# Performance work log

Hardware: AMD Instinct MI355X
Metric: run time of the kernel (lower is better)

The kernel has to match this reference:

```python
import jax, jax.numpy as jnp
import numpy as np

N_VOXELS = 262144
MAX_PTS = 32
C = 4
N_PATCHES = 2048          # total patches across the batch
VOXELS_PER_PATCH = 128    # N_PATCHES * 128 == N_VOXELS
BATCH = 4
PATCH_PER_SAMPLE = 512    # BATCH * 512 == N_PATCHES


def setup_inputs() -> dict:
    key = jax.random.key(0)
    k1, k2, k3, k4 = jax.random.split(key, 4)
    patch_voxels = jax.random.normal(k1, (N_VOXELS, MAX_PTS, C), dtype=jnp.float32)
    patch_voxel_num_points = jax.random.randint(k2, (N_VOXELS,), 0, MAX_PTS + 1, dtype=jnp.int32)
    patch_voxel_coords = jax.random.randint(k3, (N_VOXELS, 4), 0, 256, dtype=jnp.int32)
    # counts per patch; must sum to N_VOXELS (constant counts for a fixed-shape reference)
    patch_voxel_num_array = jnp.ones((N_PATCHES,), dtype=jnp.int32) * VOXELS_PER_PATCH
    valid_patch_center_array = jax.random.normal(k4, (N_PATCHES, 2), dtype=jnp.float32)
    valid_patch_num_array = jnp.ones((BATCH,), dtype=jnp.int32) * PATCH_PER_SAMPLE
    return {
        'patch_voxels': patch_voxels,
        'patch_voxel_num_points': patch_voxel_num_points,
        'patch_voxel_coords': patch_voxel_coords,
        'patch_voxel_num_array': patch_voxel_num_array,
        'valid_patch_center_array': valid_patch_center_array,
        'valid_patch_num_array': valid_patch_num_array,
    }


def reference(patch_voxels, patch_voxel_num_points, patch_voxel_coords,
              patch_voxel_num_array, valid_patch_center_array, valid_patch_num_array):
    # --- voxel mean pooling: sum over points, divide by clamped point count ---
    points_sum = patch_voxels.sum(axis=1)                                  # [N, C]
    normalizer = jnp.clip(patch_voxel_num_points.astype(patch_voxels.dtype), 1.0)[:, None]
    voxel_features = points_sum / normalizer                               # [N, C]

    # --- vectorized segment-id assignment (replaces the per-patch Python loop) ---
    # voxel j belongs to patch i where cumsum[i-1] <= j < cumsum[i]
    accu = jnp.cumsum(patch_voxel_num_array)                               # [P]
    n = patch_voxels.shape[0]
    batch_ids = jnp.searchsorted(accu, jnp.arange(n, dtype=accu.dtype), side='right')
    voxel_coords = patch_voxel_coords.at[:, 0].set(batch_ids.astype(patch_voxel_coords.dtype))

    # --- patch centers padded with z = 0 (flat array instead of per-sample list) ---
    z_pad = jnp.zeros((valid_patch_center_array.shape[0], 1), dtype=jnp.float32)
    patch_center_xyz = jnp.concatenate([valid_patch_center_array, z_pad], axis=-1)  # [V, 3]

    patch_num_list = valid_patch_num_array.astype(jnp.int32)
    return voxel_features, voxel_coords, patch_center_xyz, patch_num_list
```

## Files before the change

kernel.cpp:

```cpp
#include <hip/hip_runtime.h>


#define P_MAX 4096

__device__ __forceinline__ void reduce_store(
    float4 a0, float4 a1, float4 a2, float4 a3,
    int np, int t, int voxel, float4* __restrict__ out0)
{
    float sx = a0.x + a1.x + a2.x + a3.x;
    float sy = a0.y + a1.y + a2.y + a3.y;
    float sz = a0.z + a1.z + a2.z + a3.z;
    float sw = a0.w + a1.w + a2.w + a3.w;
#pragma unroll
    for (int m = 4; m; m >>= 1) {
        sx += __shfl_xor(sx, m);
        sy += __shfl_xor(sy, m);
        sz += __shfl_xor(sz, m);
        sw += __shfl_xor(sw, m);
    }
    if (t == 0) {
        float inv = 1.0f / fmaxf((float)np, 1.0f);
        out0[voxel] = make_float4(sx * inv, sy * inv, sz * inv, sw * inv);
    }
}

__global__ __launch_bounds__(256) void fused_pipe_kernel(
    const float4* __restrict__ pv,
    const int*    __restrict__ npts,
    const int4*   __restrict__ coords,
    const int*    __restrict__ counts,
    const float*  __restrict__ centers,
    const int*    __restrict__ nums,
    float4* __restrict__ out0,
    float4* __restrict__ out1,
    float*  __restrict__ out2,
    float*  __restrict__ out3,
    int n_voxels, int P, int V, int B,
    int coordBlocks, int ppb)
{
    __shared__ int s_accu[P_MAX];
    __shared__ int s_wsum[4];

    const int b   = blockIdx.x;
    const int tid = threadIdx.x;
    const int t   = tid & 7;
    const int g   = tid >> 3;

    const int vbase = b * 128;

    float4 a0, a1, a2, a3;
    int npA = 0;
    int v0i = vbase + g;
    bool ok0 = v0i < n_voxels;
    if (ok0) {
        const float4* base = pv + (size_t)v0i * 32;
        a0 = base[t]; a1 = base[t + 8]; a2 = base[t + 16]; a3 = base[t + 24];
        npA = npts[v0i];
    }

    if (b < coordBlocks) {
        {
            const int chunk = (P + 255) >> 8;
            const int cbeg = tid * chunk;
            const int cend = min(cbeg + chunk, P);
            int s = 0;
            for (int i = cbeg; i < cend; ++i) s += counts[i];
            const int lane = tid & 63;
            const int wave = tid >> 6;
            int acc = s;
#pragma unroll
            for (int off = 1; off < 64; off <<= 1) {
                int u = __shfl_up(acc, off);
                if (lane >= off) acc += u;
            }
            if (lane == 63) s_wsum[wave] = acc;
            __syncthreads();
            int wpre = 0;
            for (int w = 0; w < wave; ++w) wpre += s_wsum[w];
            int run = wpre + acc - s;
            for (int i = cbeg; i < cend; ++i) {
                run += counts[i];
                s_accu[i] = run;
            }
            __syncthreads();
        }
        const int pBeg = b * ppb;
        if (pBeg < P) {
            const int pEnd = min(pBeg + ppb, P);
            const int sBeg = (pBeg == 0) ? 0 : s_accu[pBeg - 1];
            const int sEnd = s_accu[pEnd - 1];
            for (int j = sBeg + tid; j < sEnd; j += 256) {
                int p = pBeg;
                while (p < pEnd - 1 && s_accu[p] <= j) ++p;
                int4 c = coords[j];
                out1[j] = make_float4((float)p, (float)c.y, (float)c.z, (float)c.w);
            }
        }
        if (b == 0) {
            for (int i = tid; i < V; i += 256) {
                out2[3 * i + 0] = centers[2 * i + 0];
                out2[3 * i + 1] = centers[2 * i + 1];
                out2[3 * i + 2] = 0.0f;
            }
            for (int i = tid; i < B; i += 256) out3[i] = (float)nums[i];
        }
    }

#pragma unroll
    for (int it = 0; it < 4; ++it) {
        float4 b0, b1, b2, b3;
        int npB = 0;
        int vNext = vbase + (it + 1) * 32 + g;
        bool okN = (it < 3) && (vNext < n_voxels);
        if (okN) {
            const float4* base = pv + (size_t)vNext * 32;
            b0 = base[t]; b1 = base[t + 8]; b2 = base[t + 16]; b3 = base[t + 24];
            npB = npts[vNext];
        }
        int vCur = vbase + it * 32 + g;
        if (vCur < n_voxels) {
            reduce_store(a0, a1, a2, a3, npA, t, vCur, out0);
        }
        a0 = b0; a1 = b1; a2 = b2; a3 = b3;
        npA = npB;
    }
}

extern "C" void kernel_launch(void* const* d_in, const int* in_sizes, int n_in,
                              void* d_out, int out_size, void* d_ws, size_t ws_size,
                              hipStream_t stream) {
    const float* pv      = (const float*)d_in[0];
    const int*   npts    = (const int*)d_in[1];
    const int*   coords  = (const int*)d_in[2];
    const int*   pcounts = (const int*)d_in[3];
    const float* centers = (const float*)d_in[4];
    const int*   vnums   = (const int*)d_in[5];

    const int N = in_sizes[1];
    const int P = in_sizes[3];
    const int V = in_sizes[4] / 2;
    const int B = in_sizes[5];

    float* out0 = (float*)d_out;
    float* out1 = out0 + (size_t)N * 4;
    float* out2 = out1 + (size_t)N * 4;
    float* out3 = out2 + (size_t)V * 3;

    const int blocks      = (N + 127) / 128;
    const int coordBlocks = 512;
    const int ppb         = (P + coordBlocks - 1) / coordBlocks;

    fused_pipe_kernel<<<blocks, 256, 0, stream>>>(
        (const float4*)pv, npts, (const int4*)coords, pcounts, centers, vnums,
        (float4*)out0, (float4*)out1, out2, out3,
        N, P, V, B, coordBlocks, ppb);
}
```

Baseline: 26.31 us.

## Spread coord segment work across all blocks with per-block prefix reduction

Instead of 512 blocks each computing a full prefix scan of patch counts into shared memory, every block now sums counts before its own patch range and handles ppb patches (one per block for this shape). Each patch's voxel range is written directly with its patch id, so the per-voxel linear search is gone. This balances coord work over all blocks and drops the 16KB shared array, which may help occupancy. The cost is that later blocks read up to P counts for their prefix sum, which grows with the block index.

```diff
diff --git a/kernel.cpp b/kernel.cpp
--- a/kernel.cpp
+++ b/kernel.cpp
@@ -1,7 +1,5 @@
 #include <hip/hip_runtime.h>
 
-
-#define P_MAX 4096
 
 __device__ __forceinline__ void reduce_store(
     float4 a0, float4 a1, float4 a2, float4 a3,
@@ -24,7 +22,7 @@
     }
 }
 
-__global__ __launch_bounds__(256) void fused_pipe_kernel(
+__global__ __launch_bounds__(256) void fused_bal_kernel(
     const float4* __restrict__ pv,
     const int*    __restrict__ npts,
     const int4*   __restrict__ coords,
@@ -35,10 +33,8 @@
     float4* __restrict__ out1,
     float*  __restrict__ out2,
     float*  __restrict__ out3,
-    int n_voxels, int P, int V, int B,
-    int coordBlocks, int ppb)
+    int n_voxels, int P, int V, int B, int ppb)
 {
-    __shared__ int s_accu[P_MAX];
     __shared__ int s_wsum[4];
 
     const int b   = blockIdx.x;
@@ -50,60 +46,46 @@
 
     float4 a0, a1, a2, a3;
     int npA = 0;
-    int v0i = vbase + g;
-    bool ok0 = v0i < n_voxels;
-    if (ok0) {
-        const float4* base = pv + (size_t)v0i * 32;
-        a0 = base[t]; a1 = base[t + 8]; a2 = base[t + 16]; a3 = base[t + 24];
-        npA = npts[v0i];
+    {
+        int v0i = vbase + g;
+        if (v0i < n_voxels) {
+            const float4* base = pv + (size_t)v0i * 32;
+            a0 = base[t]; a1 = base[t + 8]; a2 = base[t + 16]; a3 = base[t + 24];
+            npA = npts[v0i];
+        }
     }
 
-    if (b < coordBlocks) {
-        {
-            const int chunk = (P + 255) >> 8;
-            const int cbeg = tid * chunk;
-            const int cend = min(cbeg + chunk, P);
-            int s = 0;
-            for (int i = cbeg; i < cend; ++i) s += counts[i];
-            const int lane = tid & 63;
-            const int wave = tid >> 6;
-            int acc = s;
+    const int pBeg = b * ppb;
+    if (pBeg < P) {
+        const int pEnd = min(pBeg + ppb, P);
+        int s = 0;
+        for (int i = tid; i < pBeg; i += 256) s += counts[i];
+        const int lane = tid & 63;
+        const int wave = tid >> 6;
 #pragma unroll
-            for (int off = 1; off < 64; off <<= 1) {
-                int u = __shfl_up(acc, off);
-                if (lane >= off) acc += u;
+        for (int m = 32; m; m >>= 1) s += __shfl_xor(s, m);
+        if (lane == 0) s_wsum[wave] = s;
+        __syncthreads();
+        int vBeg = s_wsum[0] + s_wsum[1] + s_wsum[2] + s_wsum[3];
+
+        for (int p = pBeg; p < pEnd; ++p) {
+            int vEnd = vBeg + counts[p];
+            float pf = (float)p;
+            for (int j = vBeg + tid; j < vEnd; j += 256) {
+                int4 c = coords[j];
+                out1[j] = make_float4(pf, (float)c.y, (float)c.z, (float)c.w);
             }
-            if (lane == 63) s_wsum[wave] = acc;
-            __syncthreads();
-            int wpre = 0;
-            for (int w = 0; w < wave; ++w) wpre += s_wsum[w];
-            int run = wpre + acc - s;
-            for (int i = cbeg; i < cend; ++i) {
-                run += counts[i];
-                s_accu[i] = run;
-            }
-            __syncthreads();
+            vBeg = vEnd;
         }
-        const int pBeg = b * ppb;
-        if (pBeg < P) {
-            const int pEnd = min(pBeg + ppb, P);
-            const int sBeg = (pBeg == 0) ? 0 : s_accu[pBeg - 1];
-            const int sEnd = s_accu[pEnd - 1];
-            for (int j = sBeg + tid; j < sEnd; j += 256) {
-                int p = pBeg;
-                while (p < pEnd - 1 && s_accu[p] <= j) ++p;
-                int4 c = coords[j];
-                out1[j] = make_float4((float)p, (float)c.y, (float)c.z, (float)c.w);
-            }
+    }
+
+    if (b == 0) {
+        for (int i = tid; i < V; i += 256) {
+            out2[3 * i + 0] = centers[2 * i + 0];
+            out2[3 * i + 1] = centers[2 * i + 1];
+            out2[3 * i + 2] = 0.0f;
         }
-        if (b == 0) {
-            for (int i = tid; i < V; i += 256) {
-                out2[3 * i + 0] = centers[2 * i + 0];
-                out2[3 * i + 1] = centers[2 * i + 1];
-                out2[3 * i + 2] = 0.0f;
-            }
-            for (int i = tid; i < B; i += 256) out3[i] = (float)nums[i];
-        }
+        for (int i = tid; i < B; i += 256) out3[i] = (float)nums[i];
     }
 
 #pragma unroll
@@ -146,12 +128,11 @@
     float* out2 = out1 + (size_t)N * 4;
     float* out3 = out2 + (size_t)V * 3;
 
-    const int blocks      = (N + 127) / 128;
-    const int coordBlocks = 512;
-    const int ppb         = (P + coordBlocks - 1) / coordBlocks;
+    const int blocks = (N + 127) / 128;
+    const int ppb    = (P + blocks - 1) / blocks;
 
-    fused_pipe_kernel<<<blocks, 256, 0, stream>>>(
+    fused_bal_kernel<<<blocks, 256, 0, stream>>>(
         (const float4*)pv, npts, (const int4*)coords, pcounts, centers, vnums,
         (float4*)out0, (float4*)out1, out2, out3,
-        N, P, V, B, coordBlocks, ppb);
+        N, P, V, B, ppb);
 }
```

Measured after the change: 27.07 us. 1.03x slower.
